# Kernel tuning notes

Hardware: AMD Instinct MI355X
Metric: run time of the kernel (lower is better)

Reference implementation:

```python
import jax, jax.numpy as jnp
import numpy as np

B, S = 16, 32            # batch, cfg.feature_samples
CF, CC, H, W = 768, 512, 28, 28
NEG = 2                  # cfg.neg_samples
POS_INTRA_SHIFT, POS_INTER_SHIFT, NEG_INTER_SHIFT = 0.18, 0.12, 0.46


def _norm(t):
    # F.normalize(t, dim=1, eps=1e-10)
    n = jnp.sqrt(jnp.sum(t * t, axis=1, keepdims=True))
    return t / jnp.maximum(n, 1e-10)


def _grid_sample(img, grid):
    # torch F.grid_sample, bilinear, padding_mode='border', align_corners=True
    # img [B,C,H,W], grid [B,Hg,Wg,2] with (x,y) in [-1,1]
    Hh, Ww = img.shape[2], img.shape[3]
    x = (grid[..., 0] + 1.0) * 0.5 * (Ww - 1)
    y = (grid[..., 1] + 1.0) * 0.5 * (Hh - 1)
    x0 = jnp.floor(x); y0 = jnp.floor(y)
    wx = x - x0; wy = y - y0
    x0c = jnp.clip(x0, 0, Ww - 1).astype(jnp.int32)
    x1c = jnp.clip(x0 + 1, 0, Ww - 1).astype(jnp.int32)
    y0c = jnp.clip(y0, 0, Hh - 1).astype(jnp.int32)
    y1c = jnp.clip(y0 + 1, 0, Hh - 1).astype(jnp.int32)
    gather = jax.vmap(lambda im, yy, xx: im[:, yy, xx])  # -> [B,C,Hg,Wg]
    Ia, Ib = gather(img, y0c, x0c), gather(img, y1c, x0c)
    Ic, Id = gather(img, y0c, x1c), gather(img, y1c, x1c)
    wx = wx[:, None]; wy = wy[:, None]
    return Ia * (1 - wx) * (1 - wy) + Ib * (1 - wx) * wy + Ic * wx * (1 - wy) + Id * wx * wy


def _sample(t, coords):
    # sample(): grid_sample(t, coords.permute(0,2,1,3))
    return _grid_sample(t, jnp.transpose(coords, (0, 2, 1, 3)))


def _corr(a, b):
    return jnp.einsum('nchw,ncij->nhwij', a, b)


def _helper(f1, f2, c1, c2, shift):
    # fd computed under no_grad in torch
    fd = jax.lax.stop_gradient(_corr(_norm(f1), _norm(f2)))
    # cfg.pointwise = True
    old_mean = fd.mean()
    fd = fd - fd.mean(axis=(3, 4), keepdims=True)
    fd = fd - fd.mean() + old_mean
    cd = _corr(_norm(c1), _norm(c2))
    # cfg.zero_clamp=True, cfg.stabalize=False -> cd.clamp(0.0)
    return -jnp.maximum(cd, 0.0) * (fd - shift)


def setup_inputs() -> dict:
    key = jax.random.key(0)
    ks = jax.random.split(key, 11)
    return {
        'orig_feats': jax.random.normal(ks[0], (B, CF, H, W), jnp.float32),
        'orig_feats_pos': jax.random.normal(ks[1], (B, CF, H, W), jnp.float32),
        'orig_salience': jax.random.uniform(ks[2], (B, 224, 224), jnp.float32),
        'orig_salience_pos': jax.random.uniform(ks[3], (B, 224, 224), jnp.float32),
        'orig_code': jax.random.normal(ks[4], (B, CC, H, W), jnp.float32),
        'orig_code_pos': jax.random.normal(ks[5], (B, CC, H, W), jnp.float32),
        'depth': jax.random.uniform(ks[6], (B, 1, 224, 224), jnp.float32),
        'depth_pos': jax.random.uniform(ks[7], (B, 1, 224, 224), jnp.float32),
        'coords1': jax.random.uniform(ks[8], (B, S, S, 2), jnp.float32),
        'coords2': jax.random.uniform(ks[9], (B, S, S, 2), jnp.float32),
        'perms': jax.random.randint(ks[10], (NEG, B), 0, B, jnp.int32),
    }


def reference(orig_feats, orig_feats_pos, orig_salience, orig_salience_pos,
              orig_code, orig_code_pos, depth, depth_pos,
              coords1, coords2, perms):
    # random-coordinate branch: coords = rand(...) * 2 - 1
    c1 = coords1 * 2.0 - 1.0
    c2 = coords2 * 2.0 - 1.0
    feats = _sample(orig_feats, c1)
    code = _sample(orig_code, c1)
    feats_pos = _sample(orig_feats_pos, c2)
    code_pos = _sample(orig_code_pos, c2)

    pos_intra = _helper(feats, feats, code, code, POS_INTRA_SHIFT).mean()
    pos_inter = _helper(feats, feats_pos, code, code_pos, POS_INTER_SHIFT).mean()

    def neg_one(perm):
        feats_neg = _sample(orig_feats[perm], c2)
        code_neg = _sample(orig_code[perm], c2)
        return _helper(feats, feats_neg, code, code_neg, NEG_INTER_SHIFT).mean()

    neg_inter = jax.vmap(neg_one)(perms).mean()
    return jnp.stack([pos_intra, pos_inter, neg_inter])
```

## Files before the change

### kernel.cpp

```cpp
#include <hip/hip_runtime.h>
#include <hip/hip_bf16.h>

#define NB 16
#define NP 1024
#define CF 768
#define CC 512
#define HH 28
#define WW 28
#define HW 784
#define NTOT 16777216.0f

typedef float f32x4 __attribute__((ext_vector_type(4)));
typedef __fp16 f16x2 __attribute__((ext_vector_type(2)));
struct __align__(8) bf4 { __hip_bfloat16 a, b, c, d; };

__device__ __forceinline__ float b2f(__hip_bfloat16 h) { return __bfloat162float(h); }


__global__ void transpose_bf16_kernel(const float* __restrict__ in0,
                                      const float* __restrict__ in1,
                                      __hip_bfloat16* __restrict__ out, int C) {
  __shared__ float tile[32][33];
  int p0 = blockIdx.x * 32, c0 = blockIdx.y * 32;
  int t = blockIdx.z >> 4, b = blockIdx.z & 15;
  int tx = threadIdx.x, ty = threadIdx.y;
  const float* ib = (t == 0 ? in0 : in1) + (size_t)b * C * HW;
  __hip_bfloat16* ob = out + ((size_t)t * NB + b) * HW * C;
#pragma unroll
  for (int i = 0; i < 32; i += 8) {
    int c = c0 + ty + i, p = p0 + tx;
    if (p < HW) tile[ty + i][tx] = ib[(size_t)c * HW + p];
  }
  __syncthreads();
#pragma unroll
  for (int i = 0; i < 32; i += 8) {
    int p = p0 + ty + i, c = c0 + tx;
    if (p < HW) ob[(size_t)p * C + c] = __float2bfloat16(tile[tx][ty + i]);
  }
}

__global__ __launch_bounds__(256) void sample_pack_kernel(
    const __hip_bfloat16* __restrict__ fTb, const __hip_bfloat16* __restrict__ cTb,
    const float* __restrict__ coords1, const float* __restrict__ coords2,
    const int* __restrict__ perms,
    unsigned char* __restrict__ Fb, unsigned char* __restrict__ Cb,
    float* __restrict__ scF, float* __restrict__ scC) {
  __shared__ int offs[4][64];
  __shared__ float wts[4][64];
  __shared__ char tile[4160];

  int bb = blockIdx.y, slot = blockIdx.z;
  int tid = threadIdx.x;
  int p0 = blockIdx.x * 64;
  int pt = blockIdx.x >> 1, mh = blockIdx.x & 1;

  const float* coords = (slot == 0) ? coords1 : coords2;
  int srcidx;
  if (slot == 0)      srcidx = bb;
  else if (slot == 1) srcidx = 16 + bb;
  else if (slot == 2) srcidx = perms[bb];
  else                srcidx = perms[16 + bb];

  if (tid < 64) {
    int p = p0 + tid;
    float cx = coords[((size_t)bb * NP + p) * 2 + 0];
    float cy = coords[((size_t)bb * NP + p) * 2 + 1];
    float x = cx * (WW - 1), y = cy * (HH - 1);
    float x0f = floorf(x), y0f = floorf(y);
    float wx = x - x0f, wy = y - y0f;
    int x0 = min(max((int)x0f, 0), WW - 1);
    int x1 = min(max((int)x0f + 1, 0), WW - 1);
    int y0 = min(max((int)y0f, 0), HH - 1);
    int y1 = min(max((int)y0f + 1, 0), HH - 1);
    offs[0][tid] = y0 * WW + x0;
    offs[1][tid] = y1 * WW + x0;
    offs[2][tid] = y0 * WW + x1;
    offs[3][tid] = y1 * WW + x1;
    wts[0][tid] = (1.f - wx) * (1.f - wy);
    wts[1][tid] = (1.f - wx) * wy;
    wts[2][tid] = wx * (1.f - wy);
    wts[3][tid] = wx * wy;
  }
  __syncthreads();

  int gid = tid >> 4, l = tid & 15;
  int r = l >> 1, h4 = l & 1;

  {
    const __hip_bfloat16* base = fTb + (size_t)srcidx * HW * CF;
    float ssq[4] = {0.f, 0.f, 0.f, 0.f};
    for (int kt = 0; kt < 12; ++kt) {
#pragma unroll
      for (int j = 0; j < 4; ++j) {
        int m = j * 16 + gid;
        float4 v = {0.f, 0.f, 0.f, 0.f};
#pragma unroll
        for (int c = 0; c < 4; ++c) {
          const bf4 t4 = *((const bf4*)(base + (size_t)offs[c][m] * CF) + kt * 16 + l);
          float wv = wts[c][m];
          v.x += wv * b2f(t4.a); v.y += wv * b2f(t4.b);
          v.z += wv * b2f(t4.c); v.w += wv * b2f(t4.d);
        }
        ssq[j] += v.x * v.x + v.y * v.y + v.z * v.z + v.w * v.w;
        int w0 = __builtin_amdgcn_cvt_pk_fp8_f32(v.x, v.y, 0, false);
        int w1 = __builtin_amdgcn_cvt_pk_fp8_f32(v.z, v.w, w0, true);
        *(int*)(tile + r * 520 + m * 8 + h4 * 4) = w1;
      }
      __syncthreads();
      unsigned char* gbase = Fb +
          (((((size_t)slot * NB + bb) * 12 + kt) * 8 + pt) * 1024 + (size_t)mh * 64) * 8;
#pragma unroll
      for (int jj = 0; jj < 2; ++jj) {
        int cl = jj * 256 + tid;
        int rr = cl >> 6, mi = cl & 63;
        unsigned long long val = *(const unsigned long long*)(tile + rr * 520 + mi * 8);
        *(unsigned long long*)(gbase + (size_t)(rr * 128 + mi) * 8) = val;
      }
      __syncthreads();
    }
#pragma unroll
    for (int j = 0; j < 4; ++j) {
#pragma unroll
      for (int mm = 1; mm < 16; mm <<= 1) ssq[j] += __shfl_xor(ssq[j], mm);
    }
    if (l == 0) {
#pragma unroll
      for (int j = 0; j < 4; ++j) {
        int p = p0 + j * 16 + gid;
        scF[((size_t)slot * NB + bb) * NP + p] = 1.f / fmaxf(sqrtf(ssq[j]), 1e-10f);
      }
    }
  }

  {
    const __hip_bfloat16* base = cTb + (size_t)srcidx * HW * CC;
    float ssq[4] = {0.f, 0.f, 0.f, 0.f};
    for (int kt = 0; kt < 8; ++kt) {
#pragma unroll
      for (int j = 0; j < 4; ++j) {
        int m = j * 16 + gid;
        float4 v = {0.f, 0.f, 0.f, 0.f};
#pragma unroll
        for (int c = 0; c < 4; ++c) {
          const bf4 t4 = *((const bf4*)(base + (size_t)offs[c][m] * CC) + kt * 16 + l);
          float wv = wts[c][m];
          v.x += wv * b2f(t4.a); v.y += wv * b2f(t4.b);
          v.z += wv * b2f(t4.c); v.w += wv * b2f(t4.d);
        }
        ssq[j] += v.x * v.x + v.y * v.y + v.z * v.z + v.w * v.w;
        int w0 = __builtin_amdgcn_cvt_pk_fp8_f32(v.x, v.y, 0, false);
        int w1 = __builtin_amdgcn_cvt_pk_fp8_f32(v.z, v.w, w0, true);
        *(int*)(tile + r * 520 + m * 8 + h4 * 4) = w1;
      }
      __syncthreads();
      unsigned char* gbase = Cb +
          (((((size_t)slot * NB + bb) * 8 + kt) * 8 + pt) * 1024 + (size_t)mh * 64) * 8;
#pragma unroll
      for (int jj = 0; jj < 2; ++jj) {
        int cl = jj * 256 + tid;
        int rr = cl >> 6, mi = cl & 63;
        unsigned long long val = *(const unsigned long long*)(tile + rr * 520 + mi * 8);
        *(unsigned long long*)(gbase + (size_t)(rr * 128 + mi) * 8) = val;
      }
      __syncthreads();
    }
#pragma unroll
    for (int j = 0; j < 4; ++j) {
#pragma unroll
      for (int mm = 1; mm < 16; mm <<= 1) ssq[j] += __shfl_xor(ssq[j], mm);
    }
    if (l == 0) {
#pragma unroll
      for (int j = 0; j < 4; ++j) {
        int p = p0 + j * 16 + gid;
        scC[((size_t)slot * NB + bb) * NP + p] = 1.f / fmaxf(sqrtf(ssq[j]), 1e-10f);
      }
    }
  }
}

__device__ __forceinline__ void stage_sup(const unsigned long long* __restrict__ st,
                                          unsigned long long* buf, int tid) {
#pragma unroll
  for (int i = 0; i < 2; ++i) {
    const char* g = (const char*)st + (size_t)(i * 256 + tid) * 16;
    char* d = (char*)buf + i * 4096 + (tid & 192) * 16;
    __builtin_amdgcn_global_load_lds(
        (const __attribute__((address_space(1))) void*)g,
        (__attribute__((address_space(3))) void*)d, 16, 0, 0);
  }
}

__device__ __forceinline__ void mfma_tile(const unsigned long long* __restrict__ A,
                                          const unsigned long long* __restrict__ B,
                                          int aoff, int boff, f32x4 acc[4][4]) {
#pragma unroll
  for (int s = 0; s < 2; ++s) {
    long a[4], b[4];
#pragma unroll
    for (int mi = 0; mi < 4; ++mi) a[mi] = (long)A[s * 512 + aoff + mi * 16];
#pragma unroll
    for (int ni = 0; ni < 4; ++ni) b[ni] = (long)B[s * 512 + boff + ni * 16];
#pragma unroll
    for (int mi = 0; mi < 4; ++mi)
#pragma unroll
      for (int ni = 0; ni < 4; ++ni)
        acc[mi][ni] = __builtin_amdgcn_mfma_f32_16x16x32_fp8_fp8(
            a[mi], b[ni], acc[mi][ni], 0, 0, 0);
  }
}

#define WAITV(N) asm volatile("s_waitcnt vmcnt(" #N ")" ::: "memory")
#define BAR() do { __builtin_amdgcn_s_barrier(); \
                   __builtin_amdgcn_sched_barrier(0); } while (0)

__global__ __launch_bounds__(256, 3) void corr_kernel(
    const unsigned long long* __restrict__ Fb,
    const unsigned long long* __restrict__ Cb,
    const float* __restrict__ scF, const float* __restrict__ scC,
    float* __restrict__ rowfd, float* __restrict__ rowrcd,
    float* __restrict__ cross) {
  __shared__ unsigned long long As[3][1024], Bs[3][1024];
  __shared__ float sm[512];

  int id = blockIdx.x;
  int zl = id & 7, q = id >> 3;
  int bx = q & 7, by = (q >> 3) & 7, zh = q >> 6;
  int z = zh * 8 + zl;
  int h = z >> 4, bb = z & 15;
  int p0 = bx * 128, q0 = by * 128;
  int tid = threadIdx.x, ln = tid & 63, w = tid >> 6;
  int wm = w >> 1, wn = w & 1, quad = ln >> 4, t16 = ln & 15;
  int aoff = quad * 128 + wm * 64 + t16;
  int boff = quad * 128 + wn * 64 + t16;

  const unsigned long long* AfB = Fb + (((size_t)bb * 12) * 8 + bx) * 1024;
  const unsigned long long* BfB = Fb + ((((size_t)h * NB + bb) * 12) * 8 + by) * 1024;
  const unsigned long long* AcB = Cb + (((size_t)bb * 8) * 8 + bx) * 1024;
  const unsigned long long* BcB = Cb + ((((size_t)h * NB + bb) * 8) * 8 + by) * 1024;
  const size_t KTSTR = (size_t)8 * 1024;

  {
    const float* s0 = scF + (size_t)bb * NP;
    const float* s1 = scF + ((size_t)h * NB + bb) * NP;
    const float* s2 = scC + (size_t)bb * NP;
    const float* s3 = scC + ((size_t)h * NB + bb) * NP;
    if (tid < 128) {
      sm[tid] = s0[p0 + tid];
      sm[256 + tid] = s2[p0 + tid];
    } else {
      int u = tid - 128;
      sm[128 + u] = s1[q0 + u];
      sm[384 + u] = s3[q0 + u];
    }
  }
  asm volatile("s_waitcnt vmcnt(0) lgkmcnt(0)" ::: "memory");
  __builtin_amdgcn_sched_barrier(0);

  f32x4 acc[4][4];
#pragma unroll
  for (int i = 0; i < 4; ++i)
#pragma unroll
    for (int j = 0; j < 4; ++j) acc[i][j] = (f32x4){0.f, 0.f, 0.f, 0.f};

  stage_sup(AcB, As[0], tid);
  stage_sup(BcB, Bs[0], tid);
  stage_sup(AcB + KTSTR, As[1], tid);
  stage_sup(BcB + KTSTR, Bs[1], tid);
#pragma unroll
  for (int kt = 0; kt < 8; ++kt) {
    if (kt < 7) { WAITV(4); } else { WAITV(0); }
    BAR();
    if (kt + 2 < 8) {
      stage_sup(AcB + (size_t)(kt + 2) * KTSTR, As[(kt + 2) % 3], tid);
      stage_sup(BcB + (size_t)(kt + 2) * KTSTR, Bs[(kt + 2) % 3], tid);
    }
    __builtin_amdgcn_s_setprio(1);
    mfma_tile(As[kt % 3], Bs[kt % 3], aoff, boff, acc);
    __builtin_amdgcn_s_setprio(0);
  }

  f16x2 rcp[4][4][2];
  {
    float sbc[4];
#pragma unroll
    for (int ni = 0; ni < 4; ++ni) sbc[ni] = sm[384 + wn * 64 + ni * 16 + t16];
#pragma unroll
    for (int mi = 0; mi < 4; ++mi) {
      float sac[4], srw[4];
#pragma unroll
      for (int r = 0; r < 4; ++r) {
        sac[r] = sm[256 + wm * 64 + mi * 16 + quad * 4 + r];
        srw[r] = 0.f;
      }
#pragma unroll
      for (int ni = 0; ni < 4; ++ni) {
        float rc0 = fmaxf(acc[mi][ni][0] * (sac[0] * sbc[ni]), 0.f);
        float rc1 = fmaxf(acc[mi][ni][1] * (sac[1] * sbc[ni]), 0.f);
        float rc2 = fmaxf(acc[mi][ni][2] * (sac[2] * sbc[ni]), 0.f);
        float rc3 = fmaxf(acc[mi][ni][3] * (sac[3] * sbc[ni]), 0.f);
        srw[0] += rc0; srw[1] += rc1; srw[2] += rc2; srw[3] += rc3;
        rcp[mi][ni][0] = __builtin_amdgcn_cvt_pkrtz(rc0, rc1);
        rcp[mi][ni][1] = __builtin_amdgcn_cvt_pkrtz(rc2, rc3);
      }
#pragma unroll
      for (int r = 0; r < 4; ++r) {
#pragma unroll
        for (int mm = 1; mm < 16; mm <<= 1) srw[r] += __shfl_xor(srw[r], mm);
        if (t16 == 0) {
          int p = p0 + wm * 64 + mi * 16 + quad * 4 + r;
          atomicAdd(&rowrcd[((size_t)h * NB + bb) * NP + p], srw[r]);
        }
      }
    }
  }

#pragma unroll
  for (int i = 0; i < 4; ++i)
#pragma unroll
    for (int j = 0; j < 4; ++j) acc[i][j] = (f32x4){0.f, 0.f, 0.f, 0.f};

  __syncthreads();

  stage_sup(AfB, As[0], tid);
  stage_sup(BfB, Bs[0], tid);
  stage_sup(AfB + KTSTR, As[1], tid);
  stage_sup(BfB + KTSTR, Bs[1], tid);
#pragma unroll
  for (int kt = 0; kt < 12; ++kt) {
    if (kt < 11) { WAITV(4); } else { WAITV(0); }
    BAR();
    if (kt + 2 < 12) {
      stage_sup(AfB + (size_t)(kt + 2) * KTSTR, As[(kt + 2) % 3], tid);
      stage_sup(BfB + (size_t)(kt + 2) * KTSTR, Bs[(kt + 2) % 3], tid);
    }
    __builtin_amdgcn_s_setprio(1);
    mfma_tile(As[kt % 3], Bs[kt % 3], aoff, boff, acc);
    __builtin_amdgcn_s_setprio(0);
  }

  float cross_l = 0.f;
  {
    float sbf[4];
#pragma unroll
    for (int ni = 0; ni < 4; ++ni) sbf[ni] = sm[128 + wn * 64 + ni * 16 + t16];
#pragma unroll
    for (int mi = 0; mi < 4; ++mi) {
      float saf[4], sfd[4];
#pragma unroll
      for (int r = 0; r < 4; ++r) {
        saf[r] = sm[wm * 64 + mi * 16 + quad * 4 + r];
        sfd[r] = 0.f;
      }
#pragma unroll
      for (int ni = 0; ni < 4; ++ni) {
        float fd0 = acc[mi][ni][0] * (saf[0] * sbf[ni]);
        float fd1 = acc[mi][ni][1] * (saf[1] * sbf[ni]);
        float fd2 = acc[mi][ni][2] * (saf[2] * sbf[ni]);
        float fd3 = acc[mi][ni][3] * (saf[3] * sbf[ni]);
        sfd[0] += fd0; sfd[1] += fd1; sfd[2] += fd2; sfd[3] += fd3;
        cross_l += (float)rcp[mi][ni][0][0] * fd0;
        cross_l += (float)rcp[mi][ni][0][1] * fd1;
        cross_l += (float)rcp[mi][ni][1][0] * fd2;
        cross_l += (float)rcp[mi][ni][1][1] * fd3;
      }
#pragma unroll
      for (int r = 0; r < 4; ++r) {
#pragma unroll
        for (int mm = 1; mm < 16; mm <<= 1) sfd[r] += __shfl_xor(sfd[r], mm);
        if (t16 == 0) {
          int p = p0 + wm * 64 + mi * 16 + quad * 4 + r;
          atomicAdd(&rowfd[((size_t)h * NB + bb) * NP + p], sfd[r]);
        }
      }
    }
  }
#pragma unroll
  for (int mm = 1; mm < 64; mm <<= 1) cross_l += __shfl_xor(cross_l, mm);
  __syncthreads();
  if (ln == 0) sm[w] = cross_l;
  __syncthreads();
  if (tid == 0) atomicAdd(&cross[h], sm[0] + sm[1] + sm[2] + sm[3]);
}

__global__ void finalize_partial(const float* __restrict__ rowfd,
                                 const float* __restrict__ rowrcd,
                                 const float* __restrict__ cross,
                                 float* __restrict__ losses) {
  __shared__ float r1[16], r2[16], r3[16];
  const float shifts[4] = {0.18f, 0.12f, 0.46f, 0.46f};
  int h = blockIdx.x, tid = threadIdx.x, w = tid >> 6, ln = tid & 63;
  float s1 = 0.f, s2 = 0.f, s3 = 0.f;
  for (int i = tid; i < NB * NP; i += 1024) {
    float a = rowfd[h * NB * NP + i];
    float c = rowrcd[h * NB * NP + i];
    s1 += a;
    s2 += c;
    s3 += a * c;
  }
#pragma unroll
  for (int mm = 1; mm < 64; mm <<= 1) {
    s1 += __shfl_xor(s1, mm);
    s2 += __shfl_xor(s2, mm);
    s3 += __shfl_xor(s3, mm);
  }
  if (ln == 0) { r1[w] = s1; r2[w] = s2; r3[w] = s3; }
  __syncthreads();
  if (tid == 0) {
    float Sfd = 0.f, Srcd = 0.f, Sdot = 0.f;
#pragma unroll
    for (int i = 0; i < 16; ++i) { Sfd += r1[i]; Srcd += r2[i]; Sdot += r3[i]; }
    losses[h] = -(cross[h] - Sdot * (1.0f / 1024.0f) +
                  (Sfd / NTOT - shifts[h]) * Srcd) / NTOT;
  }
}

__global__ void finalize_combine(const float* __restrict__ losses,
                                 float* __restrict__ out) {
  if (threadIdx.x == 0) {
    out[0] = losses[0];
    out[1] = losses[1];
    out[2] = 0.5f * (losses[2] + losses[3]);
  }
}

extern "C" void kernel_launch(void* const* d_in, const int* in_sizes, int n_in,
                              void* d_out, int out_size, void* d_ws, size_t ws_size,
                              hipStream_t stream) {
  (void)in_sizes; (void)n_in; (void)out_size; (void)ws_size;
  const float* orig_feats = (const float*)d_in[0];
  const float* orig_feats_pos = (const float*)d_in[1];
  const float* orig_code = (const float*)d_in[4];
  const float* orig_code_pos = (const float*)d_in[5];
  const float* coords1 = (const float*)d_in[8];
  const float* coords2 = (const float*)d_in[9];
  const int* perms = (const int*)d_in[10];
  float* out = (float*)d_out;

  char* ws = (char*)d_ws;
  size_t off = 0;
  __hip_bfloat16* fTb = (__hip_bfloat16*)(ws + off); off += (size_t)2 * NB * HW * CF * 2;
  __hip_bfloat16* cTb = (__hip_bfloat16*)(ws + off); off += (size_t)2 * NB * HW * CC * 2;
  unsigned char* Fb = (unsigned char*)(ws + off); off += (size_t)4 * NB * NP * CF;
  unsigned char* Cb = (unsigned char*)(ws + off); off += (size_t)4 * NB * NP * CC;
  float* rowfd  = (float*)(ws + off); off += (size_t)4 * NB * NP * 4;
  float* rowrcd = (float*)(ws + off); off += (size_t)4 * NB * NP * 4;
  float* cross  = (float*)(ws + off); off += 64;
  float* losses = (float*)(ws + off); off += 64;
  float* scF    = (float*)(ws + off); off += (size_t)4 * NB * NP * 4;
  float* scC    = (float*)(ws + off); off += (size_t)4 * NB * NP * 4;

  (void)hipMemsetAsync(rowfd, 0, (size_t)4 * NB * NP * 4 * 2 + 128, stream);

  dim3 tb(32, 8);
  transpose_bf16_kernel<<<dim3(25, 24, 32), tb, 0, stream>>>(
      orig_feats, orig_feats_pos, fTb, CF);
  transpose_bf16_kernel<<<dim3(25, 16, 32), tb, 0, stream>>>(
      orig_code, orig_code_pos, cTb, CC);
  sample_pack_kernel<<<dim3(16, 16, 4), 256, 0, stream>>>(
      fTb, cTb, coords1, coords2, perms, Fb, Cb, scF, scC);

  corr_kernel<<<dim3(4096), 256, 0, stream>>>(
      (const unsigned long long*)Fb, (const unsigned long long*)Cb,
      scF, scC, rowfd, rowrcd, cross);
  finalize_partial<<<4, 1024, 0, stream>>>(rowfd, rowrcd, cross, losses);
  finalize_combine<<<1, 64, 0, stream>>>(losses, out);
}
```

Baseline: 424.0 us.

## Switch correlation GEMM to 16x16x128 scaled FP8 MFMA with fused code/feature pipeline

Replaces the 16x16x32 FP8 MFMA with the gfx950 scaled 16x16x128 f8f6f4 MFMA using unit scales, so each instruction covers four times the K depth. The two separate code and feature GEMM loops are merged into one 10-step double-buffered pipeline over two K-tiles per step. The code-correlation epilogue is handled inline at step 3, which removes the drain and restart between the two phases. Scale factors are now read straight from global memory into registers instead of staged in shared memory, and occupancy bounds drop from 3 to 2 blocks because each stage buffer is larger and fragments are held in registers.

```diff
diff --git a/kernel.cpp b/kernel.cpp
--- a/kernel.cpp
+++ b/kernel.cpp
@@ -11,8 +11,10 @@
 #define NTOT 16777216.0f
 
 typedef float f32x4 __attribute__((ext_vector_type(4)));
+typedef int i32x8 __attribute__((ext_vector_type(8)));
 typedef __fp16 f16x2 __attribute__((ext_vector_type(2)));
 struct __align__(8) bf4 { __hip_bfloat16 a, b, c, d; };
+union fragu { unsigned long long u[4]; i32x8 v; };
 
 __device__ __forceinline__ float b2f(__hip_bfloat16 h) { return __bfloat162float(h); }
 
@@ -191,37 +193,17 @@
   }
 }
 
-__device__ __forceinline__ void mfma_tile(const unsigned long long* __restrict__ A,
-                                          const unsigned long long* __restrict__ B,
-                                          int aoff, int boff, f32x4 acc[4][4]) {
-#pragma unroll
-  for (int s = 0; s < 2; ++s) {
-    long a[4], b[4];
-#pragma unroll
-    for (int mi = 0; mi < 4; ++mi) a[mi] = (long)A[s * 512 + aoff + mi * 16];
-#pragma unroll
-    for (int ni = 0; ni < 4; ++ni) b[ni] = (long)B[s * 512 + boff + ni * 16];
-#pragma unroll
-    for (int mi = 0; mi < 4; ++mi)
-#pragma unroll
-      for (int ni = 0; ni < 4; ++ni)
-        acc[mi][ni] = __builtin_amdgcn_mfma_f32_16x16x32_fp8_fp8(
-            a[mi], b[ni], acc[mi][ni], 0, 0, 0);
-  }
-}
-
 #define WAITV(N) asm volatile("s_waitcnt vmcnt(" #N ")" ::: "memory")
 #define BAR() do { __builtin_amdgcn_s_barrier(); \
                    __builtin_amdgcn_sched_barrier(0); } while (0)
 
-__global__ __launch_bounds__(256, 3) void corr_kernel(
+__global__ __launch_bounds__(256, 2) void corr_kernel(
     const unsigned long long* __restrict__ Fb,
     const unsigned long long* __restrict__ Cb,
     const float* __restrict__ scF, const float* __restrict__ scC,
     float* __restrict__ rowfd, float* __restrict__ rowrcd,
     float* __restrict__ cross) {
-  __shared__ unsigned long long As[3][1024], Bs[3][1024];
-  __shared__ float sm[512];
+  __shared__ unsigned long long As[2][2048], Bs[2][2048];
 
   int id = blockIdx.x;
   int zl = id & 7, q = id >> 3;
@@ -231,8 +213,10 @@
   int p0 = bx * 128, q0 = by * 128;
   int tid = threadIdx.x, ln = tid & 63, w = tid >> 6;
   int wm = w >> 1, wn = w & 1, quad = ln >> 4, t16 = ln & 15;
-  int aoff = quad * 128 + wm * 64 + t16;
-  int boff = quad * 128 + wn * 64 + t16;
+  int ma = wm * 64 + t16;
+  int mb = wn * 64 + t16;
+  int stq = (quad >> 1) * 1024;
+  int rb = (quad & 1) * 4;
 
   const unsigned long long* AfB = Fb + (((size_t)bb * 12) * 8 + bx) * 1024;
   const unsigned long long* BfB = Fb + ((((size_t)h * NB + bb) * 12) * 8 + by) * 1024;
@@ -240,21 +224,29 @@
   const unsigned long long* BcB = Cb + ((((size_t)h * NB + bb) * 8) * 8 + by) * 1024;
   const size_t KTSTR = (size_t)8 * 1024;
 
+#define STEPA(t) ((t) < 4 ? AcB + (size_t)(2 * (t)) * KTSTR \
+                          : AfB + (size_t)(2 * ((t) - 4)) * KTSTR)
+#define STEPB(t) ((t) < 4 ? BcB + (size_t)(2 * (t)) * KTSTR \
+                          : BfB + (size_t)(2 * ((t) - 4)) * KTSTR)
+#define STAGE(t, b) do { \
+    stage_sup(STEPA(t), As[b], tid); \
+    stage_sup(STEPA(t) + KTSTR, As[b] + 1024, tid); \
+    stage_sup(STEPB(t), Bs[b], tid); \
+    stage_sup(STEPB(t) + KTSTR, Bs[b] + 1024, tid); } while (0)
+
+  float sbc_c[4], sac_c[16];
   {
-    const float* s0 = scF + (size_t)bb * NP;
-    const float* s1 = scF + ((size_t)h * NB + bb) * NP;
-    const float* s2 = scC + (size_t)bb * NP;
-    const float* s3 = scC + ((size_t)h * NB + bb) * NP;
-    if (tid < 128) {
-      sm[tid] = s0[p0 + tid];
-      sm[256 + tid] = s2[p0 + tid];
-    } else {
-      int u = tid - 128;
-      sm[128 + u] = s1[q0 + u];
-      sm[384 + u] = s3[q0 + u];
-    }
-  }
-  asm volatile("s_waitcnt vmcnt(0) lgkmcnt(0)" ::: "memory");
+    const float* sAc = scC + (size_t)bb * NP + p0;
+    const float* sBc = scC + ((size_t)h * NB + bb) * NP + q0;
+#pragma unroll
+    for (int ni = 0; ni < 4; ++ni) sbc_c[ni] = sBc[wn * 64 + ni * 16 + t16];
+#pragma unroll
+    for (int mi = 0; mi < 4; ++mi)
+#pragma unroll
+      for (int r = 0; r < 4; ++r)
+        sac_c[mi * 4 + r] = sAc[wm * 64 + mi * 16 + quad * 4 + r];
+  }
+  asm volatile("s_waitcnt vmcnt(0)" ::: "memory");
   __builtin_amdgcn_sched_barrier(0);
 
   f32x4 acc[4][4];
@@ -263,93 +255,83 @@
 #pragma unroll
     for (int j = 0; j < 4; ++j) acc[i][j] = (f32x4){0.f, 0.f, 0.f, 0.f};
 
-  stage_sup(AcB, As[0], tid);
-  stage_sup(BcB, Bs[0], tid);
-  stage_sup(AcB + KTSTR, As[1], tid);
-  stage_sup(BcB + KTSTR, Bs[1], tid);
-#pragma unroll
-  for (int kt = 0; kt < 8; ++kt) {
-    if (kt < 7) { WAITV(4); } else { WAITV(0); }
+  f16x2 rcp[4][4][2];
+
+  STAGE(0, 0);
+  STAGE(1, 1);
+
+#pragma unroll
+  for (int t = 0; t < 10; ++t) {
+    if (t < 9) { WAITV(8); } else { WAITV(0); }
     BAR();
-    if (kt + 2 < 8) {
-      stage_sup(AcB + (size_t)(kt + 2) * KTSTR, As[(kt + 2) % 3], tid);
-      stage_sup(BcB + (size_t)(kt + 2) * KTSTR, Bs[(kt + 2) % 3], tid);
-    }
+    const unsigned long long* A = As[t & 1];
+    const unsigned long long* B = Bs[t & 1];
+    fragu fa[4], fb[4];
+#pragma unroll
+    for (int mi = 0; mi < 4; ++mi)
+#pragma unroll
+      for (int j = 0; j < 4; ++j) {
+        fa[mi].u[j] = A[stq + (rb + j) * 128 + ma + mi * 16];
+        fb[mi].u[j] = B[stq + (rb + j) * 128 + mb + mi * 16];
+      }
+    asm volatile("s_waitcnt lgkmcnt(0)" ::: "memory");
+    __builtin_amdgcn_sched_barrier(0);
+    __builtin_amdgcn_s_barrier();
+    __builtin_amdgcn_sched_barrier(0);
+    if (t + 2 < 10) STAGE(t + 2, t & 1);
     __builtin_amdgcn_s_setprio(1);
-    mfma_tile(As[kt % 3], Bs[kt % 3], aoff, boff, acc);
+#pragma unroll
+    for (int mi = 0; mi < 4; ++mi)
+#pragma unroll
+      for (int ni = 0; ni < 4; ++ni)
+        acc[mi][ni] = __builtin_amdgcn_mfma_scale_f32_16x16x128_f8f6f4(
+            fa[mi].v, fb[ni].v, acc[mi][ni], 0, 0,
+            0, 0x7F7F7F7F, 0, 0x7F7F7F7F);
     __builtin_amdgcn_s_setprio(0);
-  }
-
-  f16x2 rcp[4][4][2];
-  {
-    float sbc[4];
-#pragma unroll
-    for (int ni = 0; ni < 4; ++ni) sbc[ni] = sm[384 + wn * 64 + ni * 16 + t16];
-#pragma unroll
-    for (int mi = 0; mi < 4; ++mi) {
-      float sac[4], srw[4];
-#pragma unroll
-      for (int r = 0; r < 4; ++r) {
-        sac[r] = sm[256 + wm * 64 + mi * 16 + quad * 4 + r];
-        srw[r] = 0.f;
-      }
-#pragma unroll
-      for (int ni = 0; ni < 4; ++ni) {
-        float rc0 = fmaxf(acc[mi][ni][0] * (sac[0] * sbc[ni]), 0.f);
-        float rc1 = fmaxf(acc[mi][ni][1] * (sac[1] * sbc[ni]), 0.f);
-        float rc2 = fmaxf(acc[mi][ni][2] * (sac[2] * sbc[ni]), 0.f);
-        float rc3 = fmaxf(acc[mi][ni][3] * (sac[3] * sbc[ni]), 0.f);
-        srw[0] += rc0; srw[1] += rc1; srw[2] += rc2; srw[3] += rc3;
-        rcp[mi][ni][0] = __builtin_amdgcn_cvt_pkrtz(rc0, rc1);
-        rcp[mi][ni][1] = __builtin_amdgcn_cvt_pkrtz(rc2, rc3);
-      }
-#pragma unroll
-      for (int r = 0; r < 4; ++r) {
-#pragma unroll
-        for (int mm = 1; mm < 16; mm <<= 1) srw[r] += __shfl_xor(srw[r], mm);
-        if (t16 == 0) {
-          int p = p0 + wm * 64 + mi * 16 + quad * 4 + r;
-          atomicAdd(&rowrcd[((size_t)h * NB + bb) * NP + p], srw[r]);
+    if (t == 3) {
+#pragma unroll
+      for (int mi = 0; mi < 4; ++mi) {
+        float srw[4] = {0.f, 0.f, 0.f, 0.f};
+#pragma unroll
+        for (int ni = 0; ni < 4; ++ni) {
+          float rc0 = fmaxf(acc[mi][ni][0] * (sac_c[mi * 4 + 0] * sbc_c[ni]), 0.f);
+          float rc1 = fmaxf(acc[mi][ni][1] * (sac_c[mi * 4 + 1] * sbc_c[ni]), 0.f);
+          float rc2 = fmaxf(acc[mi][ni][2] * (sac_c[mi * 4 + 2] * sbc_c[ni]), 0.f);
+          float rc3 = fmaxf(acc[mi][ni][3] * (sac_c[mi * 4 + 3] * sbc_c[ni]), 0.f);
+          srw[0] += rc0; srw[1] += rc1; srw[2] += rc2; srw[3] += rc3;
+          rcp[mi][ni][0] = __builtin_amdgcn_cvt_pkrtz(rc0, rc1);
+          rcp[mi][ni][1] = __builtin_amdgcn_cvt_pkrtz(rc2, rc3);
         }
-      }
-    }
-  }
-
-#pragma unroll
-  for (int i = 0; i < 4; ++i)
-#pragma unroll
-    for (int j = 0; j < 4; ++j) acc[i][j] = (f32x4){0.f, 0.f, 0.f, 0.f};
-
-  __syncthreads();
-
-  stage_sup(AfB, As[0], tid);
-  stage_sup(BfB, Bs[0], tid);
-  stage_sup(AfB + KTSTR, As[1], tid);
-  stage_sup(BfB + KTSTR, Bs[1], tid);
-#pragma unroll
-  for (int kt = 0; kt < 12; ++kt) {
-    if (kt < 11) { WAITV(4); } else { WAITV(0); }
-    BAR();
-    if (kt + 2 < 12) {
-      stage_sup(AfB + (size_t)(kt + 2) * KTSTR, As[(kt + 2) % 3], tid);
-      stage_sup(BfB + (size_t)(kt + 2) * KTSTR, Bs[(kt + 2) % 3], tid);
-    }
-    __builtin_amdgcn_s_setprio(1);
-    mfma_tile(As[kt % 3], Bs[kt % 3], aoff, boff, acc);
-    __builtin_amdgcn_s_setprio(0);
+#pragma unroll
+        for (int r = 0; r < 4; ++r) {
+#pragma unroll
+          for (int mm = 1; mm < 16; mm <<= 1) srw[r] += __shfl_xor(srw[r], mm);
+          if (t16 == 0) {
+            int p = p0 + wm * 64 + mi * 16 + quad * 4 + r;
+            atomicAdd(&rowrcd[((size_t)h * NB + bb) * NP + p], srw[r]);
+          }
+        }
+      }
+#pragma unroll
+      for (int i = 0; i < 4; ++i)
+#pragma unroll
+        for (int j = 0; j < 4; ++j) acc[i][j] = (f32x4){0.f, 0.f, 0.f, 0.f};
+    }
   }
 
   float cross_l = 0.f;
   {
+    const float* sAf = scF + (size_t)bb * NP + p0;
+    const float* sBf = scF + ((size_t)h * NB + bb) * NP + q0;
     float sbf[4];
 #pragma unroll
-    for (int ni = 0; ni < 4; ++ni) sbf[ni] = sm[128 + wn * 64 + ni * 16 + t16];
+    for (int ni = 0; ni < 4; ++ni) sbf[ni] = sBf[wn * 64 + ni * 16 + t16];
 #pragma unroll
     for (int mi = 0; mi < 4; ++mi) {
       float saf[4], sfd[4];
 #pragma unroll
       for (int r = 0; r < 4; ++r) {
-        saf[r] = sm[wm * 64 + mi * 16 + quad * 4 + r];
+        saf[r] = sAf[wm * 64 + mi * 16 + quad * 4 + r];
         sfd[r] = 0.f;
       }
 #pragma unroll
@@ -378,9 +360,13 @@
 #pragma unroll
   for (int mm = 1; mm < 64; mm <<= 1) cross_l += __shfl_xor(cross_l, mm);
   __syncthreads();
-  if (ln == 0) sm[w] = cross_l;
+  float* crs = (float*)As;
+  if (ln == 0) crs[w] = cross_l;
   __syncthreads();
-  if (tid == 0) atomicAdd(&cross[h], sm[0] + sm[1] + sm[2] + sm[3]);
+  if (tid == 0) atomicAdd(&cross[h], crs[0] + crs[1] + crs[2] + crs[3]);
+#undef STAGE
+#undef STEPA
+#undef STEPB
 }
 
 __global__ void finalize_partial(const float* __restrict__ rowfd,
```

Result: slower. 928.8 us (+119.0%).
